# Performance work log

Hardware: AMD Instinct MI355X
Metric: run time of the kernel (lower is better)

The kernel has to match this reference:

```python
import jax, jax.numpy as jnp
import numpy as np


def setup_inputs() -> dict:
    key = jax.random.key(0)
    ks = jax.random.split(key, 10)
    B, T = 64, 2048
    inp_p, inp_q, out = 512, 512, 512
    def xavier(k, shape):
        fan_in, fan_out = shape[1], shape[0]
        limit = np.sqrt(6.0 / (fan_in + fan_out))
        return jax.random.uniform(k, shape, jnp.float32, -limit, limit)
    return {
        "input_p": jax.random.normal(ks[0], (B, inp_p), jnp.float32),
        "input_q": jax.random.normal(ks[1], (B, T, inp_q), jnp.float32),
        "h_tm1": jax.random.normal(ks[2], (B, out), jnp.float32),
        "Wp": xavier(ks[3], (out, inp_p)),
        "bp": jnp.zeros((out,), jnp.float32),
        "Wq": xavier(ks[4], (out, inp_q)),
        "bq": jnp.zeros((out,), jnp.float32),
        "Wr": xavier(ks[5], (out, out)),
        "br": jnp.zeros((out,), jnp.float32),
        "w": 0.05 * jax.random.normal(ks[6], (out,), jnp.float32),
        "match_b": jnp.ones((1,), jnp.float32),
        "depth": 0,
    }


def reference(input_p, input_q, h_tm1, Wp, bp, Wq, bq, Wr, br, w, match_b, depth):
    # depth selects the layer; single layer (depth=0) parameters provided.
    G_p = (input_p @ Wp.T + bp)[:, None, :]          # [B, 1, out]
    G_q = jnp.einsum("btq,oq->bto", input_q, Wq) + bq  # [B, T, out]
    G_r = (h_tm1 @ Wr.T + br)[:, None, :]            # [B, 1, out]
    G = jnp.tanh(G_p + G_q + G_r)                    # [B, T, out]
    alpha = jnp.einsum("bto,o->bt", G, w) + match_b[0]  # [B, T]
    alpha = jax.nn.softmax(alpha, axis=-1)
    z = jnp.einsum("bt,btq->bq", alpha, input_q)     # [B, inp_q]
    return jnp.concatenate([input_p, z], axis=1)     # [B, inp_p+inp_q]
```

## Files before the change

kernel.cpp:

```cpp
#include <hip/hip_runtime.h>
#include <stdint.h>
#include <stddef.h>


#define B_ 64
#define T_ 2048
#define D_ 512

typedef __attribute__((ext_vector_type(8))) short short8;
typedef __attribute__((ext_vector_type(4))) unsigned short ushort4v;
typedef __attribute__((ext_vector_type(8))) unsigned short ushort8v;
typedef __attribute__((ext_vector_type(4))) float f32x4;

__device__ __forceinline__ unsigned short f2bf(float f) {
    unsigned int u = __builtin_bit_cast(unsigned int, f);
    return (unsigned short)((u + 0x7FFFu + ((u >> 16) & 1u)) >> 16);
}

__global__ __launch_bounds__(256) void k_convert(const float* __restrict__ Wq,
                                                 unsigned short* __restrict__ Wq_bf) {
    int i = (blockIdx.x * 256 + threadIdx.x) * 8;
    float4 a = *(const float4*)(Wq + i);
    float4 b = *(const float4*)(Wq + i + 4);
    ushort8v o;
    o[0] = f2bf(a.x); o[1] = f2bf(a.y); o[2] = f2bf(a.z); o[3] = f2bf(a.w);
    o[4] = f2bf(b.x); o[5] = f2bf(b.y); o[6] = f2bf(b.z); o[7] = f2bf(b.w);
    *(ushort8v*)(Wq_bf + i) = o;
}

__global__ __launch_bounds__(256) void k_prq(
        const float* __restrict__ ip, const float* __restrict__ h,
        const float* __restrict__ Wp, const float* __restrict__ Wr,
        const float* __restrict__ bp, const float* __restrict__ bq,
        const float* __restrict__ br, float* __restrict__ prq) {
    __shared__ float ip_lds[64][68];
    __shared__ float h_lds[64][68];
    __shared__ float wp_lds[8][68];
    __shared__ float wr_lds[8][68];
    const int tid = threadIdx.x;
    const int o0 = blockIdx.x * 8;
    const int bb = tid >> 3;
    const int oo = tid & 7;
    float acc0 = 0.f, acc1 = 0.f;
    const int lrow = tid >> 2;
    const int lcol = (tid & 3) * 16;
    for (int kc = 0; kc < 512; kc += 64) {
        #pragma unroll
        for (int j = 0; j < 16; j += 4) {
            float4 v = *(const float4*)(ip + lrow * 512 + kc + lcol + j);
            ip_lds[lrow][lcol + j] = v.x; ip_lds[lrow][lcol + j + 1] = v.y;
            ip_lds[lrow][lcol + j + 2] = v.z; ip_lds[lrow][lcol + j + 3] = v.w;
            float4 u = *(const float4*)(h + lrow * 512 + kc + lcol + j);
            h_lds[lrow][lcol + j] = u.x; h_lds[lrow][lcol + j + 1] = u.y;
            h_lds[lrow][lcol + j + 2] = u.z; h_lds[lrow][lcol + j + 3] = u.w;
        }
        if (tid < 128) {
            int r = tid >> 4, c = (tid & 15) * 4;
            float4 v = *(const float4*)(Wp + (size_t)(o0 + r) * 512 + kc + c);
            wp_lds[r][c] = v.x; wp_lds[r][c + 1] = v.y; wp_lds[r][c + 2] = v.z; wp_lds[r][c + 3] = v.w;
        } else {
            int t2 = tid - 128;
            int r = t2 >> 4, c = (t2 & 15) * 4;
            float4 v = *(const float4*)(Wr + (size_t)(o0 + r) * 512 + kc + c);
            wr_lds[r][c] = v.x; wr_lds[r][c + 1] = v.y; wr_lds[r][c + 2] = v.z; wr_lds[r][c + 3] = v.w;
        }
        __syncthreads();
        #pragma unroll 4
        for (int k = 0; k < 64; ++k) {
            float wpv = wp_lds[oo][k], wrv = wr_lds[oo][k];
            acc0 += ip_lds[bb][k] * wpv + h_lds[bb][k] * wrv;
            acc1 += ip_lds[bb + 32][k] * wpv + h_lds[bb + 32][k] * wrv;
        }
        __syncthreads();
    }
    const int o = o0 + oo;
    float base = bp[o] + bq[o] + br[o];
    prq[bb * 512 + o] = acc0 + base;
    prq[(bb + 32) * 512 + o] = acc1 + base;
}

__global__ __launch_bounds__(512, 1) void k_gq(
        const float* __restrict__ iq, const unsigned short* __restrict__ Wq_bf,
        const float* __restrict__ prq, const float* __restrict__ wv,
        const float* __restrict__ match_b, float* __restrict__ logits) {
    __shared__ unsigned short A_t[64][32];
    __shared__ unsigned short B_t[512][32];
    __shared__ float w_lds[512];
    __shared__ float prq_lds[512];
    __shared__ float red[4][64];

    const int tid = threadIdx.x;
    const int m0 = blockIdx.x * 64;
    const int b = m0 >> 11;
    w_lds[tid] = wv[tid];
    prq_lds[tid] = prq[b * 512 + tid];

    const int lane = tid & 63;
    const int wave = tid >> 6;
    const int wm = wave >> 2;
    const int wn = wave & 3;
    const int r16 = lane & 15;
    const int cc = lane >> 4;

    f32x4 acc[2][8];
    #pragma unroll
    for (int i = 0; i < 2; ++i)
        #pragma unroll
        for (int j = 0; j < 8; ++j) acc[i][j] = (f32x4){0.f, 0.f, 0.f, 0.f};

    const int arow = tid >> 3;
    const int koff = (tid & 7) * 4;
    const int adst = (((koff >> 3) ^ ((arow >> 1) & 3)) << 3) + (koff & 7);
    const float* aptr = iq + (size_t)(m0 + arow) * 512 + koff;

    const int aro0 = wm * 32 + r16;
    const int aro1 = aro0 + 16;
    const int aofs0 = ((cc ^ ((aro0 >> 1) & 3)) << 3);
    const int aofs1 = ((cc ^ ((aro1 >> 1) & 3)) << 3);

    for (int k0 = 0; k0 < 512; k0 += 32) {
        float4 av = *(const float4*)(aptr + k0);
        ushort4v ap;
        ap[0] = f2bf(av.x); ap[1] = f2bf(av.y); ap[2] = f2bf(av.z); ap[3] = f2bf(av.w);
        *(ushort4v*)&A_t[arow][adst] = ap;
        #pragma unroll
        for (int i = 0; i < 4; ++i) {
            int task = i * 512 + tid;
            int brow = task >> 2;
            int bch = task & 3;
            short8 v = *(const short8*)(Wq_bf + (size_t)brow * 512 + k0 + bch * 8);
            *(short8*)&B_t[brow][((bch ^ ((brow >> 1) & 3)) << 3)] = v;
        }
        __syncthreads();
        short8 a0 = *(const short8*)&A_t[aro0][aofs0];
        short8 a1 = *(const short8*)&A_t[aro1][aofs1];
        #pragma unroll
        for (int nf = 0; nf < 8; ++nf) {
            int brow = wn * 128 + nf * 16 + r16;
            short8 bfr = *(const short8*)&B_t[brow][((cc ^ ((brow >> 1) & 3)) << 3)];
            acc[0][nf] = __builtin_amdgcn_mfma_f32_16x16x32_bf16(a0, bfr, acc[0][nf], 0, 0, 0);
            acc[1][nf] = __builtin_amdgcn_mfma_f32_16x16x32_bf16(a1, bfr, acc[1][nf], 0, 0, 0);
        }
        __syncthreads();
    }

    float part[2][4];
    #pragma unroll
    for (int mf = 0; mf < 2; ++mf)
        #pragma unroll
        for (int j = 0; j < 4; ++j) part[mf][j] = 0.f;

    #pragma unroll
    for (int nf = 0; nf < 8; ++nf) {
        int c = wn * 128 + nf * 16 + r16;
        float wc = w_lds[c];
        float pc = prq_lds[c];
        #pragma unroll
        for (int mf = 0; mf < 2; ++mf) {
            #pragma unroll
            for (int j = 0; j < 4; ++j) {
                float x = acc[mf][nf][j] + pc;
                float e = __expf(2.f * x);
                float g = 1.f - 2.f / (e + 1.f);
                part[mf][j] += wc * g;
            }
        }
    }
    #pragma unroll
    for (int mf = 0; mf < 2; ++mf)
        #pragma unroll
        for (int j = 0; j < 4; ++j) {
            float v = part[mf][j];
            v += __shfl_xor(v, 1);
            v += __shfl_xor(v, 2);
            v += __shfl_xor(v, 4);
            v += __shfl_xor(v, 8);
            part[mf][j] = v;
        }
    if (r16 == 0) {
        int rg = (lane >> 4) * 4;
        #pragma unroll
        for (int mf = 0; mf < 2; ++mf)
            #pragma unroll
            for (int j = 0; j < 4; ++j)
                red[wn][wm * 32 + mf * 16 + rg + j] = part[mf][j];
    }
    __syncthreads();
    if (tid < 64) {
        float l = red[0][tid] + red[1][tid] + red[2][tid] + red[3][tid] + match_b[0];
        logits[m0 + tid] = l;
    }
}

__global__ __launch_bounds__(256) void k_stats(const float* __restrict__ logits,
                                               const float* __restrict__ ip,
                                               float* __restrict__ out,
                                               float* __restrict__ stats) {
    const int b = blockIdx.x, tid = threadIdx.x;
    __shared__ float sm[256];
    float m = -1e30f;
    for (int i = tid; i < 2048; i += 256) m = fmaxf(m, logits[b * 2048 + i]);
    sm[tid] = m;
    __syncthreads();
    for (int s = 128; s > 0; s >>= 1) {
        if (tid < s) sm[tid] = fmaxf(sm[tid], sm[tid + s]);
        __syncthreads();
    }
    float bmax = sm[0];
    __syncthreads();
    float ssum = 0.f;
    for (int i = tid; i < 2048; i += 256) ssum += __expf(logits[b * 2048 + i] - bmax);
    sm[tid] = ssum;
    __syncthreads();
    for (int s = 128; s > 0; s >>= 1) {
        if (tid < s) sm[tid] += sm[tid + s];
        __syncthreads();
    }
    if (tid == 0) { stats[b * 2] = bmax; stats[b * 2 + 1] = sm[0]; }
    out[b * 1024 + tid] = ip[b * 512 + tid];
    out[b * 1024 + 256 + tid] = ip[b * 512 + 256 + tid];
    out[b * 1024 + 512 + tid] = 0.f;
    out[b * 1024 + 768 + tid] = 0.f;
}

#define NC 16
#define TC 128
__global__ __launch_bounds__(256) void k_z(const float* __restrict__ logits,
                                           const float* __restrict__ stats,
                                           const float* __restrict__ iq,
                                           float* __restrict__ out) {
    const int blk = blockIdx.x;
    const int b = blk >> 4;
    const int c = blk & 15;
    const int tid = threadIdx.x;
    __shared__ float al[TC];
    const float bmax = stats[b * 2];
    const float inv = 1.f / stats[b * 2 + 1];
    if (tid < TC) al[tid] = __expf(logits[b * 2048 + c * TC + tid] - bmax) * inv;
    __syncthreads();
    const int q = tid * 2;
    float ax = 0.f, ay = 0.f;
    const float* base = iq + ((size_t)b * 2048 + (size_t)c * TC) * 512 + q;
    #pragma unroll 4
    for (int t = 0; t < TC; ++t) {
        float2 v = *(const float2*)(base + (size_t)t * 512);
        float a = al[t];
        ax += a * v.x;
        ay += a * v.y;
    }
    atomicAdd(&out[b * 1024 + 512 + q], ax);
    atomicAdd(&out[b * 1024 + 512 + q + 1], ay);
}

extern "C" void kernel_launch(void* const* d_in, const int* in_sizes, int n_in,
                              void* d_out, int out_size, void* d_ws, size_t ws_size,
                              hipStream_t stream) {
    const float* input_p = (const float*)d_in[0];
    const float* input_q = (const float*)d_in[1];
    const float* h_tm1   = (const float*)d_in[2];
    const float* Wp      = (const float*)d_in[3];
    const float* bp      = (const float*)d_in[4];
    const float* Wq      = (const float*)d_in[5];
    const float* bq      = (const float*)d_in[6];
    const float* Wr      = (const float*)d_in[7];
    const float* br      = (const float*)d_in[8];
    const float* wv      = (const float*)d_in[9];
    const float* match_b = (const float*)d_in[10];
    float* out = (float*)d_out;

    char* ws = (char*)d_ws;
    unsigned short* Wq_bf = (unsigned short*)ws;
    float* prq    = (float*)(ws + 512 * 1024);
    float* logits = (float*)(ws + 640 * 1024);
    float* stats  = (float*)(ws + 1152 * 1024);

    k_convert<<<dim3(128), dim3(256), 0, stream>>>(Wq, Wq_bf);
    k_prq<<<dim3(64), dim3(256), 0, stream>>>(input_p, h_tm1, Wp, Wr, bp, bq, br, prq);
    k_gq<<<dim3(2048), dim3(512), 0, stream>>>(input_q, Wq_bf, prq, wv, match_b, logits);
    k_stats<<<dim3(64), dim3(256), 0, stream>>>(logits, input_p, out, stats);
    k_z<<<dim3(64 * 16), dim3(256), 0, stream>>>(logits, stats, input_q, out);
}
```

Before: 201.7 us.

## Fuse logits, softmax partials and weighted sum into GEMM kernel with async B prefetch

The attention-logit GEMM kernel now keeps the whole 64x512 input_q tile in LDS as bf16 and computes per-tile softmax max/sum plus a partial weighted sum z directly, so the separate stats and z kernels that re-read input_q (256 MB fp32) are removed. A small combine kernel merges the 32 partials per batch with log-sum-exp rescaling. The Wq tile is double-buffered via global_load_lds with manual waitcnt/barrier pipelining, and occupancy is raised to 2 blocks per CU. The z reduction now uses bf16-rounded input_q, which loses some precision, and match_b is dropped because a constant shift cancels in softmax.

```diff
diff --git a/kernel.cpp b/kernel.cpp
--- a/kernel.cpp
+++ b/kernel.cpp
@@ -1,14 +1,10 @@
 #include <hip/hip_runtime.h>
+#include <hip/hip_bf16.h>
 #include <stdint.h>
 #include <stddef.h>
 
 
-#define B_ 64
-#define T_ 2048
-#define D_ 512
-
 typedef __attribute__((ext_vector_type(8))) short short8;
-typedef __attribute__((ext_vector_type(4))) unsigned short ushort4v;
 typedef __attribute__((ext_vector_type(8))) unsigned short ushort8v;
 typedef __attribute__((ext_vector_type(4))) float f32x4;
 
@@ -17,15 +13,33 @@
     return (unsigned short)((u + 0x7FFFu + ((u >> 16) & 1u)) >> 16);
 }
 
-__global__ __launch_bounds__(256) void k_convert(const float* __restrict__ Wq,
-                                                 unsigned short* __restrict__ Wq_bf) {
-    int i = (blockIdx.x * 256 + threadIdx.x) * 8;
-    float4 a = *(const float4*)(Wq + i);
-    float4 b = *(const float4*)(Wq + i + 4);
-    ushort8v o;
-    o[0] = f2bf(a.x); o[1] = f2bf(a.y); o[2] = f2bf(a.z); o[3] = f2bf(a.w);
-    o[4] = f2bf(b.x); o[5] = f2bf(b.y); o[6] = f2bf(b.z); o[7] = f2bf(b.w);
-    *(ushort8v*)(Wq_bf + i) = o;
+__device__ __forceinline__ uint2 cvt4(float4 a) {
+    union { __hip_bfloat162 h[2]; uint2 v; } u;
+    u.h[0] = __float22bfloat162_rn(make_float2(a.x, a.y));
+    u.h[1] = __float22bfloat162_rn(make_float2(a.z, a.w));
+    return u.v;
+}
+
+__device__ __forceinline__ float bf2f(unsigned short u) {
+    unsigned v = (unsigned)u << 16;
+    return __builtin_bit_cast(float, v);
+}
+
+__device__ __forceinline__ void gload_lds16(const void* g, void* l) {
+    __builtin_amdgcn_global_load_lds(
+        (const __attribute__((address_space(1))) unsigned int*)g,
+        (__attribute__((address_space(3))) unsigned int*)l, 16, 0, 0);
+}
+
+__global__ __launch_bounds__(256) void k_convert8(const float* __restrict__ src,
+                                                  unsigned short* __restrict__ dst) {
+    size_t i = ((size_t)blockIdx.x * 256 + threadIdx.x) * 8;
+    float4 a = *(const float4*)(src + i);
+    float4 b = *(const float4*)(src + i + 4);
+    uint2 lo = cvt4(a), hi = cvt4(b);
+    union { uint2 u[2]; short8 s; } p;
+    p.u[0] = lo; p.u[1] = hi;
+    *(short8*)(dst + i) = p.s;
 }
 
 __global__ __launch_bounds__(256) void k_prq(
@@ -79,19 +93,24 @@
     prq[(bb + 32) * 512 + o] = acc1 + base;
 }
 
-__global__ __launch_bounds__(512, 1) void k_gq(
+union ZB { unsigned short B[2][16384]; float zp[8][512]; };
+
+__global__ __launch_bounds__(512, 2) void k_fused(
         const float* __restrict__ iq, const unsigned short* __restrict__ Wq_bf,
         const float* __restrict__ prq, const float* __restrict__ wv,
-        const float* __restrict__ match_b, float* __restrict__ logits) {
-    __shared__ unsigned short A_t[64][32];
-    __shared__ unsigned short B_t[512][32];
+        float* __restrict__ zp_g, float* __restrict__ ms_g) {
+    __shared__ unsigned short A_p[16][2064];
+    __shared__ ZB sB;
     __shared__ float w_lds[512];
     __shared__ float prq_lds[512];
     __shared__ float red[4][64];
+    __shared__ float e_lds[64];
 
     const int tid = threadIdx.x;
-    const int m0 = blockIdx.x * 64;
-    const int b = m0 >> 11;
+    const int bid = blockIdx.x;
+    const int m0 = bid * 64;
+    const int b = bid >> 5;
+
     w_lds[tid] = wv[tid];
     prq_lds[tid] = prq[b * 512 + tid];
 
@@ -101,6 +120,30 @@
     const int wn = wave & 3;
     const int r16 = lane & 15;
     const int cc = lane >> 4;
+    const int swz = ((cc ^ ((r16 >> 1) & 3)) << 3);
+
+    const int arow = tid >> 3;
+    const int afg = tid & 7;
+    const float* asrc = iq + (size_t)(m0 + arow) * 512 + afg * 4;
+    const int adst_off = arow * 32 + ((((afg >> 1)) ^ ((arow >> 1) & 3)) << 3) + (afg & 1) * 4;
+
+    const unsigned short *bsrc0, *bsrc1, *bsrc2, *bsrc3;
+    {
+        int c0 = tid,        r0 = c0 >> 2, s0 = (c0 & 3) ^ ((r0 >> 1) & 3);
+        int c1 = 512 + tid,  r1 = c1 >> 2, s1 = (c1 & 3) ^ ((r1 >> 1) & 3);
+        int c2 = 1024 + tid, r2 = c2 >> 2, s2 = (c2 & 3) ^ ((r2 >> 1) & 3);
+        int c3 = 1536 + tid, r3 = c3 >> 2, s3 = (c3 & 3) ^ ((r3 >> 1) & 3);
+        bsrc0 = Wq_bf + (size_t)r0 * 512 + (s0 << 3);
+        bsrc1 = Wq_bf + (size_t)r1 * 512 + (s1 << 3);
+        bsrc2 = Wq_bf + (size_t)r2 * 512 + (s2 << 3);
+        bsrc3 = Wq_bf + (size_t)r3 * 512 + (s3 << 3);
+    }
+
+#define BSTAGE(KT, BUF)                                                             \
+    gload_lds16(bsrc0 + (KT) * 32, (char*)&sB.B[BUF][0] + 0 * 8192 + wave * 1024);  \
+    gload_lds16(bsrc1 + (KT) * 32, (char*)&sB.B[BUF][0] + 1 * 8192 + wave * 1024);  \
+    gload_lds16(bsrc2 + (KT) * 32, (char*)&sB.B[BUF][0] + 2 * 8192 + wave * 1024);  \
+    gload_lds16(bsrc3 + (KT) * 32, (char*)&sB.B[BUF][0] + 3 * 8192 + wave * 1024);
 
     f32x4 acc[2][8];
     #pragma unroll
@@ -108,41 +151,53 @@
         #pragma unroll
         for (int j = 0; j < 8; ++j) acc[i][j] = (f32x4){0.f, 0.f, 0.f, 0.f};
 
-    const int arow = tid >> 3;
-    const int koff = (tid & 7) * 4;
-    const int adst = (((koff >> 3) ^ ((arow >> 1) & 3)) << 3) + (koff & 7);
-    const float* aptr = iq + (size_t)(m0 + arow) * 512 + koff;
-
-    const int aro0 = wm * 32 + r16;
-    const int aro1 = aro0 + 16;
-    const int aofs0 = ((cc ^ ((aro0 >> 1) & 3)) << 3);
-    const int aofs1 = ((cc ^ ((aro1 >> 1) & 3)) << 3);
-
-    for (int k0 = 0; k0 < 512; k0 += 32) {
-        float4 av = *(const float4*)(aptr + k0);
-        ushort4v ap;
-        ap[0] = f2bf(av.x); ap[1] = f2bf(av.y); ap[2] = f2bf(av.z); ap[3] = f2bf(av.w);
-        *(ushort4v*)&A_t[arow][adst] = ap;
-        #pragma unroll
-        for (int i = 0; i < 4; ++i) {
-            int task = i * 512 + tid;
-            int brow = task >> 2;
-            int bch = task & 3;
-            short8 v = *(const short8*)(Wq_bf + (size_t)brow * 512 + k0 + bch * 8);
-            *(short8*)&B_t[brow][((bch ^ ((brow >> 1) & 3)) << 3)] = v;
-        }
-        __syncthreads();
-        short8 a0 = *(const short8*)&A_t[aro0][aofs0];
-        short8 a1 = *(const short8*)&A_t[aro1][aofs1];
-        #pragma unroll
-        for (int nf = 0; nf < 8; ++nf) {
-            int brow = wn * 128 + nf * 16 + r16;
-            short8 bfr = *(const short8*)&B_t[brow][((cc ^ ((brow >> 1) & 3)) << 3)];
-            acc[0][nf] = __builtin_amdgcn_mfma_f32_16x16x32_bf16(a0, bfr, acc[0][nf], 0, 0, 0);
-            acc[1][nf] = __builtin_amdgcn_mfma_f32_16x16x32_bf16(a1, bfr, acc[1][nf], 0, 0, 0);
-        }
-        __syncthreads();
-    }
+    float4 raA, raB;
+
+    raA = *(const float4*)(asrc);
+    BSTAGE(0, 0);
+    asm volatile("s_waitcnt vmcnt(4)" ::: "memory");
+    *(uint2*)&A_p[0][adst_off] = cvt4(raA);
+    asm volatile("s_waitcnt lgkmcnt(0)" ::: "memory");
+    __builtin_amdgcn_s_barrier();
+    raA = *(const float4*)(asrc + 32);
+    BSTAGE(1, 1);
+    asm volatile("s_waitcnt vmcnt(5)" ::: "memory");
+    __builtin_amdgcn_s_barrier();
+
+#define ITER(KT, RC, RN)                                                                  \
+    {                                                                                     \
+        const unsigned short* Ab = &A_p[KT][0];                                           \
+        const unsigned short* Bb = &sB.B[(KT) & 1][0];                                    \
+        short8 af0 = *(const short8*)&Ab[(wm * 32 + r16) * 32 + swz];                     \
+        short8 af1 = *(const short8*)&Ab[(wm * 32 + 16 + r16) * 32 + swz];                \
+        _Pragma("unroll")                                                                 \
+        for (int nf = 0; nf < 8; ++nf) {                                                  \
+            short8 bfr = *(const short8*)&Bb[(wn * 128 + nf * 16 + r16) * 32 + swz];      \
+            acc[0][nf] = __builtin_amdgcn_mfma_f32_16x16x32_bf16(af0, bfr, acc[0][nf], 0, 0, 0); \
+            acc[1][nf] = __builtin_amdgcn_mfma_f32_16x16x32_bf16(af1, bfr, acc[1][nf], 0, 0, 0); \
+        }                                                                                 \
+        if ((KT) < 15) {                                                                  \
+            asm volatile("s_waitcnt vmcnt(4)" ::: "memory");     \
+            *(uint2*)&A_p[(KT) + 1][adst_off] = cvt4(RC);                                 \
+            asm volatile("s_waitcnt lgkmcnt(0)" ::: "memory");                            \
+            __builtin_amdgcn_s_barrier();       \
+            if ((KT) < 14) {                                                              \
+                RN = *(const float4*)(asrc + ((KT) + 2) * 32);                            \
+                BSTAGE((KT) + 2, (KT) & 1);                                               \
+                asm volatile("s_waitcnt vmcnt(5)" ::: "memory");      \
+            } else {                                                                      \
+                asm volatile("s_waitcnt vmcnt(0)" ::: "memory");                          \
+            }                                                                             \
+            __builtin_amdgcn_s_barrier();                                                 \
+        }                                                                                 \
+    }
+
+    for (int kt = 0; kt < 16; kt += 2) {
+        ITER(kt, raA, raB);
+        ITER(kt + 1, raB, raA);
+    }
+#undef ITER
+#undef BSTAGE
 
     float part[2][4];
     #pragma unroll
@@ -161,8 +216,7 @@
             for (int j = 0; j < 4; ++j) {
                 float x = acc[mf][nf][j] + pc;
                 float e = __expf(2.f * x);
-                float g = 1.f - 2.f / (e + 1.f);
-                part[mf][j] += wc * g;
+                part[mf][j] += wc * (1.f - 2.f / (e + 1.f));
             }
         }
     }
@@ -178,78 +232,76 @@
             part[mf][j] = v;
         }
     if (r16 == 0) {
-        int rg = (lane >> 4) * 4;
         #pragma unroll
         for (int mf = 0; mf < 2; ++mf)
             #pragma unroll
             for (int j = 0; j < 4; ++j)
-                red[wn][wm * 32 + mf * 16 + rg + j] = part[mf][j];
-    }
-    __syncthreads();
+                red[wn][wm * 32 + mf * 16 + cc * 4 + j] = part[mf][j];
+    }
+    __syncthreads();
+
     if (tid < 64) {
-        float l = red[0][tid] + red[1][tid] + red[2][tid] + red[3][tid] + match_b[0];
-        logits[m0 + tid] = l;
-    }
-}
-
-__global__ __launch_bounds__(256) void k_stats(const float* __restrict__ logits,
-                                               const float* __restrict__ ip,
-                                               float* __restrict__ out,
-                                               float* __restrict__ stats) {
+        float l = red[0][tid] + red[1][tid] + red[2][tid] + red[3][tid];
+        float m = l;
+        #pragma unroll
+        for (int d = 1; d < 64; d <<= 1) m = fmaxf(m, __shfl_xor(m, d));
+        float ev = __expf(l - m);
+        float s = ev;
+        #pragma unroll
+        for (int d = 1; d < 64; d <<= 1) s += __shfl_xor(s, d);
+        e_lds[tid] = ev;
+        if (tid == 0) { ms_g[bid * 2] = m; ms_g[bid * 2 + 1] = s; }
+    }
+    __syncthreads();
+
+    const int q0 = (tid & 63) * 8;
+    const int kt_q = q0 >> 5;
+    const int ec = (q0 >> 3) & 3;
+    float zq[8];
+    #pragma unroll
+    for (int k = 0; k < 8; ++k) zq[k] = 0.f;
+    #pragma unroll
+    for (int ti = 0; ti < 8; ++ti) {
+        int t = (tid >> 6) * 8 + ti;
+        float ev = e_lds[t];
+        short8 av = *(const short8*)&A_p[kt_q][t * 32 + ((ec ^ ((t >> 1) & 3)) << 3)];
+        #pragma unroll
+        for (int k = 0; k < 8; ++k) zq[k] += ev * bf2f((unsigned short)av[k]);
+    }
+    __syncthreads();
+    float* zrow = &sB.zp[tid >> 6][0];
+    *(float4*)&zrow[q0]     = make_float4(zq[0], zq[1], zq[2], zq[3]);
+    *(float4*)&zrow[q0 + 4] = make_float4(zq[4], zq[5], zq[6], zq[7]);
+    __syncthreads();
+    float z = 0.f;
+    #pragma unroll
+    for (int w = 0; w < 8; ++w) z += sB.zp[w][tid];
+    zp_g[(size_t)bid * 512 + tid] = z;
+}
+
+__global__ __launch_bounds__(512) void k_comb(const float* __restrict__ zp,
+                                              const float* __restrict__ ms,
+                                              const float* __restrict__ ip,
+                                              float* __restrict__ out) {
     const int b = blockIdx.x, tid = threadIdx.x;
-    __shared__ float sm[256];
-    float m = -1e30f;
-    for (int i = tid; i < 2048; i += 256) m = fmaxf(m, logits[b * 2048 + i]);
-    sm[tid] = m;
-    __syncthreads();
-    for (int s = 128; s > 0; s >>= 1) {
-        if (tid < s) sm[tid] = fmaxf(sm[tid], sm[tid + s]);
-        __syncthreads();
-    }
-    float bmax = sm[0];
-    __syncthreads();
-    float ssum = 0.f;
-    for (int i = tid; i < 2048; i += 256) ssum += __expf(logits[b * 2048 + i] - bmax);
-    sm[tid] = ssum;
-    __syncthreads();
-    for (int s = 128; s > 0; s >>= 1) {
-        if (tid < s) sm[tid] += sm[tid + s];
-        __syncthreads();
-    }
-    if (tid == 0) { stats[b * 2] = bmax; stats[b * 2 + 1] = sm[0]; }
+    __shared__ float mm[32], ssv[32];
+    if (tid < 32) {
+        mm[tid] = ms[(b * 32 + tid) * 2];
+        ssv[tid] = ms[(b * 32 + tid) * 2 + 1];
+    }
+    __syncthreads();
+    float M = -1e30f;
+    #pragma unroll
+    for (int i = 0; i < 32; ++i) M = fmaxf(M, mm[i]);
+    float S = 0.f, z = 0.f;
+    #pragma unroll 4
+    for (int i = 0; i < 32; ++i) {
+        float sc = __expf(mm[i] - M);
+        S += ssv[i] * sc;
+        z += sc * zp[(size_t)(b * 32 + i) * 512 + tid];
+    }
+    out[b * 1024 + 512 + tid] = z / S;
     out[b * 1024 + tid] = ip[b * 512 + tid];
-    out[b * 1024 + 256 + tid] = ip[b * 512 + 256 + tid];
-    out[b * 1024 + 512 + tid] = 0.f;
-    out[b * 1024 + 768 + tid] = 0.f;
-}
-
-#define NC 16
-#define TC 128
-__global__ __launch_bounds__(256) void k_z(const float* __restrict__ logits,
-                                           const float* __restrict__ stats,
-                                           const float* __restrict__ iq,
-                                           float* __restrict__ out) {
-    const int blk = blockIdx.x;
-    const int b = blk >> 4;
-    const int c = blk & 15;
-    const int tid = threadIdx.x;
-    __shared__ float al[TC];
-    const float bmax = stats[b * 2];
-    const float inv = 1.f / stats[b * 2 + 1];
-    if (tid < TC) al[tid] = __expf(logits[b * 2048 + c * TC + tid] - bmax) * inv;
-    __syncthreads();
-    const int q = tid * 2;
-    float ax = 0.f, ay = 0.f;
-    const float* base = iq + ((size_t)b * 2048 + (size_t)c * TC) * 512 + q;
-    #pragma unroll 4
-    for (int t = 0; t < TC; ++t) {
-        float2 v = *(const float2*)(base + (size_t)t * 512);
-        float a = al[t];
-        ax += a * v.x;
-        ay += a * v.y;
-    }
-    atomicAdd(&out[b * 1024 + 512 + q], ax);
-    atomicAdd(&out[b * 1024 + 512 + q + 1], ay);
 }
 
 extern "C" void kernel_launch(void* const* d_in, const int* in_sizes, int n_in,
@@ -265,18 +317,16 @@
     const float* Wr      = (const float*)d_in[7];
     const float* br      = (const float*)d_in[8];
     const float* wv      = (const float*)d_in[9];
-    const float* match_b = (const float*)d_in[10];
     float* out = (float*)d_out;
 
     char* ws = (char*)d_ws;
     unsigned short* Wq_bf = (unsigned short*)ws;
-    float* prq    = (float*)(ws + 512 * 1024);
-    float* logits = (float*)(ws + 640 * 1024);
-    float* stats  = (float*)(ws + 1152 * 1024);
-
-    k_convert<<<dim3(128), dim3(256), 0, stream>>>(Wq, Wq_bf);
+    float* prq  = (float*)(ws + 512 * 1024);
+    float* ms   = (float*)(ws + 640 * 1024);
+    float* zp   = (float*)(ws + 1024 * 1024);
+
+    k_convert8<<<dim3(128), dim3(256), 0, stream>>>(Wq, Wq_bf);
     k_prq<<<dim3(64), dim3(256), 0, stream>>>(input_p, h_tm1, Wp, Wr, bp, bq, br, prq);
-    k_gq<<<dim3(2048), dim3(512), 0, stream>>>(input_q, Wq_bf, prq, wv, match_b, logits);
-    k_stats<<<dim3(64), dim3(256), 0, stream>>>(logits, input_p, out, stats);
-    k_z<<<dim3(64 * 16), dim3(256), 0, stream>>>(logits, stats, input_q, out);
-}
+    k_fused<<<dim3(2048), dim3(512), 0, stream>>>(input_q, Wq_bf, prq, wv, zp, ms);
+    k_comb<<<dim3(64), dim3(512), 0, stream>>>(zp, ms, input_p, out);
+}
```

Result: slower. 224.3 us (+11.2%).
